# Kernel optimization log

Measured on AMD Instinct MI355X. Metric: run time of the kernel, lower is better.

The kernel has to match this reference:

```python
import jax, jax.numpy as jnp
import numpy as np

B, L = 32768, 2048
MARGIN = 0.1

def setup_inputs() -> dict:
    key = jax.random.key(0)
    k1, k2, k3 = jax.random.split(key, 3)
    scores = jax.random.normal(k1, (B, L), dtype=jnp.float32)
    # ragged candidate lengths in [0, L]; zeros are skipped samples
    candidate_lengths = jax.random.randint(k2, (B,), 0, L + 1, dtype=jnp.int32).astype(jnp.int64)
    # at most one positive per row: a random index; it only lands inside the
    # valid region for some rows, naturally mixing pos/no-pos samples
    pos_idx = jax.random.randint(k3, (B,), 0, L, dtype=jnp.int32)
    labels = (jnp.arange(L, dtype=jnp.int32)[None, :] == pos_idx[:, None]).astype(jnp.int64)
    return {"scores": scores, "candidate_lengths": candidate_lengths, "labels": labels}

def reference(scores, candidate_lengths, labels):
    B_, L_ = scores.shape
    valid = jnp.arange(L_)[None, :] < candidate_lengths[:, None]          # [B, L]
    pos_mask = (labels == 1) & valid
    neg_mask = (labels == 0) & valid
    has_pos = jnp.any(pos_mask, axis=-1)                                   # label.sum() > 0
    has_neg = jnp.any(neg_mask, axis=-1)
    # single positive score per row (0 if none), then the -margin fallback
    pos_score = jnp.sum(jnp.where(pos_mask, scores, 0.0), axis=-1)         # [B]
    chosen = jnp.where(has_pos, pos_score, -MARGIN)                        # [B]
    hinge = jnp.maximum(MARGIN + scores - chosen[:, None], 0.0)           # [B, L]
    neg_cnt = jnp.sum(neg_mask, axis=-1)
    per_sample = jnp.sum(jnp.where(neg_mask, hinge, 0.0), axis=-1) / jnp.maximum(neg_cnt, 1).astype(scores.dtype)
    valid_obs = (candidate_lengths > 0) & has_neg
    n_valid = jnp.sum(valid_obs).astype(scores.dtype)
    total = jnp.sum(jnp.where(valid_obs, per_sample, 0.0))
    return jnp.where(n_valid > 0, total / jnp.maximum(n_valid, 1.0), 0.0)
```

## Files before the change

### kernel.cpp

```cpp
#include <hip/hip_runtime.h>


constexpr int L_DIM = 2048;
constexpr float MARGIN = 0.1f;
constexpr int NBUCKET = 1024;

__global__ __launch_bounds__(256) void hinge_row_kernel(
    const float* __restrict__ scores,
    const int*   __restrict__ lens,
    const int*   __restrict__ labels,
    float* __restrict__ acc_sum,
    float* __restrict__ acc_cnt)
{
    const int row = blockIdx.x;
    int len = lens[row];
    if (len <= 0) return;
    if (len > L_DIM) len = L_DIM;

    const int t = threadIdx.x;
    const size_t base = (size_t)row * L_DIM;
    const float4* s4 = reinterpret_cast<const float4*>(scores + base);
    const int4*   l4 = reinterpret_cast<const int4*>(labels + base);

    float sc[8];
    unsigned negmask = 0;
    float pos_local = 0.f;
    float haspos_local = 0.f;

    #pragma unroll
    for (int k = 0; k < 2; ++k) {
        const int v = t + k * 256;
        const int j = v * 4;
        if (j < len) {
            const float4 sv = s4[v];
            const int4   lv = l4[v];
            const float se[4] = {sv.x, sv.y, sv.z, sv.w};
            const int    le[4] = {lv.x, lv.y, lv.z, lv.w};
            #pragma unroll
            for (int e = 0; e < 4; ++e) {
                const int jj = j + e;
                if (jj < len) {
                    if (le[e] == 1) { pos_local += se[e]; haspos_local = 1.f; }
                    else            { sc[k * 4 + e] = se[e];
                                      negmask |= 1u << (k * 4 + e); }
                }
            }
        }
    }

    float a = pos_local, b = haspos_local;
    #pragma unroll
    for (int off = 32; off > 0; off >>= 1) {
        a += __shfl_down(a, off, 64);
        b += __shfl_down(b, off, 64);
    }
    __shared__ float red_a[4], red_b[4];
    const int wave = t >> 6;
    const int lane = t & 63;
    if (lane == 0) { red_a[wave] = a; red_b[wave] = b; }
    __syncthreads();
    const float pos_score = red_a[0] + red_a[1] + red_a[2] + red_a[3];
    const float has_pos   = red_b[0] + red_b[1] + red_b[2] + red_b[3];

    const float chosen = (has_pos > 0.f) ? pos_score : -MARGIN;

    float hsum = 0.f, hcnt = 0.f;
    #pragma unroll
    for (int i = 0; i < 8; ++i) {
        if (negmask & (1u << i)) {
            hsum += fmaxf(MARGIN + sc[i] - chosen, 0.f);
            hcnt += 1.f;
        }
    }
    #pragma unroll
    for (int off = 32; off > 0; off >>= 1) {
        hsum += __shfl_down(hsum, off, 64);
        hcnt += __shfl_down(hcnt, off, 64);
    }
    __shared__ float red_h[4], red_c[4];
    if (lane == 0) { red_h[wave] = hsum; red_c[wave] = hcnt; }
    __syncthreads();
    if (t == 0) {
        const float H = red_h[0] + red_h[1] + red_h[2] + red_h[3];
        const float C = red_c[0] + red_c[1] + red_c[2] + red_c[3];
        if (C > 0.f) {
            atomicAdd(&acc_sum[row & (NBUCKET - 1)], H / C);
            atomicAdd(&acc_cnt[row & (NBUCKET - 1)], 1.f);
        }
    }
}

__global__ __launch_bounds__(1024) void finalize_kernel(
    const float* __restrict__ acc_sum,
    const float* __restrict__ acc_cnt,
    float* __restrict__ out)
{
    const int t = threadIdx.x;
    float s = acc_sum[t];
    float c = acc_cnt[t];
    #pragma unroll
    for (int off = 32; off > 0; off >>= 1) {
        s += __shfl_down(s, off, 64);
        c += __shfl_down(c, off, 64);
    }
    __shared__ float sh_s[16], sh_c[16];
    const int wave = t >> 6, lane = t & 63;
    if (lane == 0) { sh_s[wave] = s; sh_c[wave] = c; }
    __syncthreads();
    if (t == 0) {
        float S = 0.f, C = 0.f;
        #pragma unroll
        for (int i = 0; i < 16; ++i) { S += sh_s[i]; C += sh_c[i]; }
        out[0] = (C > 0.f) ? (S / C) : 0.f;
    }
}

extern "C" void kernel_launch(void* const* d_in, const int* in_sizes, int n_in,
                              void* d_out, int out_size, void* d_ws, size_t ws_size,
                              hipStream_t stream) {
    const float* scores = (const float*)d_in[0];
    const int*   lens   = (const int*)d_in[1];
    const int*   labels = (const int*)d_in[2];
    const int B = in_sizes[1];

    float* acc_sum = (float*)d_ws;
    float* acc_cnt = acc_sum + NBUCKET;

    hipMemsetAsync(d_ws, 0, 2 * NBUCKET * sizeof(float), stream);

    hinge_row_kernel<<<B, 256, 0, stream>>>(scores, lens, labels, acc_sum, acc_cnt);
    finalize_kernel<<<1, NBUCKET, 0, stream>>>(acc_sum, acc_cnt, (float*)d_out);
}
```

Measured before the change: 456.4 us.

## Assign one wavefront per row and drop block-level shared-memory reductions

Each 64-lane wavefront now handles a whole row, with four rows per 256-thread block. All reductions use xor shuffles within the wave, so the __syncthreads barriers and LDS staging go away. Loads stop early once past the row's ragged length. Each lane now holds up to 32 scores in registers, which raises register pressure, and per-wave memory parallelism per row is lower.

```diff
diff --git a/kernel.cpp b/kernel.cpp
--- a/kernel.cpp
+++ b/kernel.cpp
@@ -4,89 +4,78 @@
 constexpr int L_DIM = 2048;
 constexpr float MARGIN = 0.1f;
 constexpr int NBUCKET = 1024;
+constexpr int WPB = 4;
 
 __global__ __launch_bounds__(256) void hinge_row_kernel(
     const float* __restrict__ scores,
     const int*   __restrict__ lens,
     const int*   __restrict__ labels,
+    int B,
     float* __restrict__ acc_sum,
     float* __restrict__ acc_cnt)
 {
-    const int row = blockIdx.x;
-    int len = lens[row];
+    const int t    = threadIdx.x;
+    const int wave = t >> 6;
+    const int lane = t & 63;
+    const int row  = blockIdx.x * WPB + wave;
+    if (row >= B) return;
+
+    int len = __builtin_amdgcn_readfirstlane(lens[row]);
     if (len <= 0) return;
     if (len > L_DIM) len = L_DIM;
 
-    const int t = threadIdx.x;
     const size_t base = (size_t)row * L_DIM;
     const float4* s4 = reinterpret_cast<const float4*>(scores + base);
     const int4*   l4 = reinterpret_cast<const int4*>(labels + base);
 
-    float sc[8];
+    float se[32];
     unsigned negmask = 0;
-    float pos_local = 0.f;
-    float haspos_local = 0.f;
+    float pos_local = 0.f, haspos_local = 0.f;
 
     #pragma unroll
-    for (int k = 0; k < 2; ++k) {
-        const int v = t + k * 256;
+    for (int k = 0; k < 8; ++k) {
+        if (k * 256 >= len) break;
+        const int v = k * 64 + lane;
         const int j = v * 4;
         if (j < len) {
             const float4 sv = s4[v];
             const int4   lv = l4[v];
-            const float se[4] = {sv.x, sv.y, sv.z, sv.w};
-            const int    le[4] = {lv.x, lv.y, lv.z, lv.w};
+            const float sve[4] = {sv.x, sv.y, sv.z, sv.w};
+            const int    lve[4] = {lv.x, lv.y, lv.z, lv.w};
             #pragma unroll
             for (int e = 0; e < 4; ++e) {
-                const int jj = j + e;
-                if (jj < len) {
-                    if (le[e] == 1) { pos_local += se[e]; haspos_local = 1.f; }
-                    else            { sc[k * 4 + e] = se[e];
-                                      negmask |= 1u << (k * 4 + e); }
+                if (j + e < len) {
+                    if (lve[e] == 1) { pos_local += sve[e]; haspos_local = 1.f; }
+                    else             { se[k * 4 + e] = sve[e];
+                                       negmask |= 1u << (k * 4 + e); }
                 }
             }
         }
     }
 
-    float a = pos_local, b = haspos_local;
     #pragma unroll
-    for (int off = 32; off > 0; off >>= 1) {
-        a += __shfl_down(a, off, 64);
-        b += __shfl_down(b, off, 64);
+    for (int off = 1; off < 64; off <<= 1) {
+        pos_local    += __shfl_xor(pos_local, off, 64);
+        haspos_local += __shfl_xor(haspos_local, off, 64);
     }
-    __shared__ float red_a[4], red_b[4];
-    const int wave = t >> 6;
-    const int lane = t & 63;
-    if (lane == 0) { red_a[wave] = a; red_b[wave] = b; }
-    __syncthreads();
-    const float pos_score = red_a[0] + red_a[1] + red_a[2] + red_a[3];
-    const float has_pos   = red_b[0] + red_b[1] + red_b[2] + red_b[3];
-
-    const float chosen = (has_pos > 0.f) ? pos_score : -MARGIN;
+    const float chosen = (haspos_local > 0.f) ? pos_local : -MARGIN;
 
     float hsum = 0.f, hcnt = 0.f;
     #pragma unroll
-    for (int i = 0; i < 8; ++i) {
+    for (int i = 0; i < 32; ++i) {
         if (negmask & (1u << i)) {
-            hsum += fmaxf(MARGIN + sc[i] - chosen, 0.f);
+            hsum += fmaxf(MARGIN + se[i] - chosen, 0.f);
             hcnt += 1.f;
         }
     }
     #pragma unroll
-    for (int off = 32; off > 0; off >>= 1) {
-        hsum += __shfl_down(hsum, off, 64);
-        hcnt += __shfl_down(hcnt, off, 64);
+    for (int off = 1; off < 64; off <<= 1) {
+        hsum += __shfl_xor(hsum, off, 64);
+        hcnt += __shfl_xor(hcnt, off, 64);
     }
-    __shared__ float red_h[4], red_c[4];
-    if (lane == 0) { red_h[wave] = hsum; red_c[wave] = hcnt; }
-    __syncthreads();
-    if (t == 0) {
-        const float H = red_h[0] + red_h[1] + red_h[2] + red_h[3];
-        const float C = red_c[0] + red_c[1] + red_c[2] + red_c[3];
-        if (C > 0.f) {
-            atomicAdd(&acc_sum[row & (NBUCKET - 1)], H / C);
-            atomicAdd(&acc_cnt[row & (NBUCKET - 1)], 1.f);
-        }
+    if (lane == 0 && hcnt > 0.f) {
+        atomicAdd(&acc_sum[row & (NBUCKET - 1)], hsum / hcnt);
+        atomicAdd(&acc_cnt[row & (NBUCKET - 1)], 1.f);
     }
 }
 
@@ -128,6 +117,8 @@
 
     hipMemsetAsync(d_ws, 0, 2 * NBUCKET * sizeof(float), stream);
 
-    hinge_row_kernel<<<B, 256, 0, stream>>>(scores, lens, labels, acc_sum, acc_cnt);
+    const int grid = (B + WPB - 1) / WPB;
+    hinge_row_kernel<<<grid, 256, 0, stream>>>(scores, lens, labels, B,
+                                               acc_sum, acc_cnt);
     finalize_kernel<<<1, NBUCKET, 0, stream>>>(acc_sum, acc_cnt, (float*)d_out);
 }
```

New measurement: 462.9 us. About the same (+1.4%).
